# Kernel optimization log

Measured on AMD Instinct MI355X. Metric: run time of the kernel, lower is better.

The kernel has to match this reference:

```python
import jax, jax.numpy as jnp
import numpy as np

BATCH = 2048
DIM = 4096
TEMPERATURE = 0.5
KD_T = 1.0
KD_WEIGHT = 1.0


def setup_inputs() -> dict:
    key = jax.random.key(0)
    k1, k2 = jax.random.split(key)
    emb_target = jax.random.normal(k1, (BATCH, DIM), dtype=jnp.float32)
    emb_surrogate = jax.random.normal(k2, (BATCH, DIM), dtype=jnp.float32)
    return {"emb_target": emb_target, "emb_surrogate": emb_surrogate}


def reference(emb_target, emb_surrogate):
    B = emb_target.shape[0]
    # --- NT-Xent contrastive loss ---
    reps = jnp.concatenate([emb_target, emb_surrogate], axis=0)  # [2B, D]
    # cosine similarity via normalized matmul (eps matches torch cosine_similarity clamp)
    norms = jnp.maximum(jnp.linalg.norm(reps, axis=1, keepdims=True), 1e-8)
    z = reps / norms
    sim = z @ z.T  # [2B, 2B]
    idx = jnp.arange(2 * B)
    # positives: diag offsets +B and -B -> sim[i, (i+B) mod 2B]
    positives = sim[idx, (idx + B) % (2 * B)]  # [2B]
    nominator = jnp.exp(positives / TEMPERATURE)
    neg_mask = 1.0 - jnp.eye(2 * B, dtype=sim.dtype)
    denominator = jnp.sum(neg_mask * jnp.exp(sim / TEMPERATURE), axis=1)  # [2B]
    cont_loss = jnp.sum(-jnp.log(nominator / denominator)) / (2 * B)
    # --- KD softmax-KL ---
    soft_targets = jax.nn.softmax(emb_target / KD_T, axis=-1)
    soft_prob = jax.nn.log_softmax(emb_surrogate / KD_T, axis=-1)
    kd_loss = jnp.sum(soft_targets * (jnp.log(soft_targets) - soft_prob)) / B * KD_T ** 2
    # --- MSE ---
    mse = jnp.mean((emb_surrogate - emb_target) ** 2)
    return cont_loss + KD_WEIGHT * kd_loss + mse
```

## Files before the change

### kernel.cpp

```cpp
#include <hip/hip_runtime.h>
#include <hip/hip_bf16.h>

#define TWO_B 4096
#define DIM_ 4096

typedef __attribute__((ext_vector_type(8))) short bf16x8;
typedef __attribute__((ext_vector_type(4))) float f32x4;
typedef __attribute__((ext_vector_type(4))) int i32x4;

static __device__ __forceinline__ unsigned short f2bf(float x) {
    return __builtin_bit_cast(unsigned short, __float2bfloat16(x));
}

static __device__ __forceinline__ float waveReduceSum(float v) {
    v += __shfl_xor(v, 1);  v += __shfl_xor(v, 2);  v += __shfl_xor(v, 4);
    v += __shfl_xor(v, 8);  v += __shfl_xor(v, 16); v += __shfl_xor(v, 32);
    return v;
}
static __device__ __forceinline__ float waveReduceMax(float v) {
    v = fmaxf(v, __shfl_xor(v, 1));  v = fmaxf(v, __shfl_xor(v, 2));
    v = fmaxf(v, __shfl_xor(v, 4));  v = fmaxf(v, __shfl_xor(v, 8));
    v = fmaxf(v, __shfl_xor(v, 16)); v = fmaxf(v, __shfl_xor(v, 32));
    return v;
}

__global__ __launch_bounds__(256) void row_stats(
    const float* __restrict__ et, const float* __restrict__ es,
    float* __restrict__ rinv, float* __restrict__ qs,
    float* __restrict__ kdp, float* __restrict__ msep,
    float* __restrict__ rowsum, char* __restrict__ z8)
{
    const int b = blockIdx.x;
    const int tid = threadIdx.x;
    const int wid = tid >> 6;

    if (b < 16) rowsum[b * 256 + tid] = 0.f;

    const float4* tp = (const float4*)(et + (size_t)b * DIM_);
    const float4* sp = (const float4*)(es + (size_t)b * DIM_);
    float4 tv[4], sv[4];
#pragma unroll
    for (int i = 0; i < 4; ++i) { tv[i] = tp[tid + 256 * i]; sv[i] = sp[tid + 256 * i]; }

    float mt = -1e30f, ms = -1e30f, amt = 0.f, ams = 0.f;
    float nt2 = 0.f, ns2 = 0.f, msev = 0.f;
#pragma unroll
    for (int i = 0; i < 4; ++i) {
        const float* tx = (const float*)&tv[i];
        const float* sx = (const float*)&sv[i];
#pragma unroll
        for (int j = 0; j < 4; ++j) {
            float a = tx[j], c = sx[j];
            mt = fmaxf(mt, a); ms = fmaxf(ms, c);
            amt = fmaxf(amt, fabsf(a)); ams = fmaxf(ams, fabsf(c));
            nt2 += a * a; ns2 += c * c;
            float d = c - a; msev += d * d;
        }
    }
    mt = waveReduceMax(mt); ms = waveReduceMax(ms);
    amt = waveReduceMax(amt); ams = waveReduceMax(ams);
    __shared__ float smx[4], sms[4], sat[4], sas[4];
    if ((tid & 63) == 0) { smx[wid] = mt; sms[wid] = ms; sat[wid] = amt; sas[wid] = ams; }
    __syncthreads();
    mt = fmaxf(fmaxf(smx[0], smx[1]), fmaxf(smx[2], smx[3]));
    ms = fmaxf(fmaxf(sms[0], sms[1]), fmaxf(sms[2], sms[3]));
    const float maT = fmaxf(fmaxf(fmaxf(sat[0], sat[1]), fmaxf(sat[2], sat[3])), 1e-20f);
    const float maS = fmaxf(fmaxf(fmaxf(sas[0], sas[1]), fmaxf(sas[2], sas[3])), 1e-20f);

    float se_t = 0.f, st = 0.f, sx_ = 0.f, se_s = 0.f;
#pragma unroll
    for (int i = 0; i < 4; ++i) {
        const float* tx = (const float*)&tv[i];
        const float* sx = (const float*)&sv[i];
#pragma unroll
        for (int j = 0; j < 4; ++j) {
            float a = tx[j], c = sx[j];
            float e = __expf(a - mt);
            se_t += e; st += e * a; sx_ += e * c;
            se_s += __expf(c - ms);
        }
    }
    float v0 = waveReduceSum(se_t), v1 = waveReduceSum(st), v2 = waveReduceSum(sx_);
    float v3 = waveReduceSum(se_s), v4 = waveReduceSum(nt2), v5 = waveReduceSum(ns2);
    float v6 = waveReduceSum(msev);
    __shared__ float sred[7][4];
    if ((tid & 63) == 0) {
        sred[0][wid] = v0; sred[1][wid] = v1; sred[2][wid] = v2; sred[3][wid] = v3;
        sred[4][wid] = v4; sred[5][wid] = v5; sred[6][wid] = v6;
    }
    __syncthreads();
    const float rT = sred[4][0] + sred[4][1] + sred[4][2] + sred[4][3];
    const float rS = sred[5][0] + sred[5][1] + sred[5][2] + sred[5][3];
    const float rinvT = 1.f / fmaxf(sqrtf(rT), 1e-8f);
    const float rinvS = 1.f / fmaxf(sqrtf(rS), 1e-8f);

    if (tid == 0) {
        float r0 = sred[0][0] + sred[0][1] + sred[0][2] + sred[0][3];
        float r1 = sred[1][0] + sred[1][1] + sred[1][2] + sred[1][3];
        float r2 = sred[2][0] + sred[2][1] + sred[2][2] + sred[2][3];
        float r3 = sred[3][0] + sred[3][1] + sred[3][2] + sred[3][3];
        float r6 = sred[6][0] + sred[6][1] + sred[6][2] + sred[6][3];
        float lse_t = mt + logf(r0);
        float lse_s = ms + logf(r3);
        kdp[b]  = (r1 - r2) / r0 - lse_t + lse_s;
        msep[b] = r6;
        rinv[b]        = rinvT;
        rinv[b + 2048] = rinvS;
        qs[b]          = maT * rinvT * (1.f / 127.f);
        qs[b + 2048]   = maS * rinvS * (1.f / 127.f);
    }

    if (z8) {
        char* zt = z8 + (size_t)b * DIM_;
        char* zs = z8 + (size_t)(b + 2048) * DIM_;
        const float fT = 127.f / maT, fS = 127.f / maS;
#pragma unroll
        for (int i = 0; i < 4; ++i) {
            const float* tx = (const float*)&tv[i];
            const float* sx = (const float*)&sv[i];
            int pt = 0, ps = 0;
#pragma unroll
            for (int j = 0; j < 4; ++j) {
                int qt = __float2int_rn(tx[j] * fT) & 0xff;
                int qv = __float2int_rn(sx[j] * fS) & 0xff;
                pt |= qt << (8 * j);
                ps |= qv << (8 * j);
            }
            ((int*)zt)[tid + 256 * i] = pt;
            ((int*)zs)[tid + 256 * i] = ps;
        }
    }
}

__global__ __launch_bounds__(256, 2) void cont_gemm12(
    const char* __restrict__ z8, const float* __restrict__ qs,
    float* __restrict__ rowsum, float* __restrict__ pos)
{
    const int bid = blockIdx.x;
    int t = (bid & 7) * 66 + (bid >> 3);
    int bi = 0;
    while (t >= (32 - bi)) { t -= (32 - bi); ++bi; }
    const int bj = bi + t;
    const int brow = bi * 128, bcol = bj * 128;
    const bool dg = (bi == bj);

    __shared__ char As[128 * 128];
    __shared__ char Bs[128 * 128];

    const int tid = threadIdx.x;
    const int lane = tid & 63;
    const int wid = tid >> 6;
    const int wm = wid >> 1, wn = wid & 1;
    const int lrow = lane >> 3;
    const int lblk = lane & 7;

    const char* srcA[4];
    const char* srcB[4];
#pragma unroll
    for (int i = 0; i < 4; ++i) {
        int r = wid * 32 + i * 8 + lrow;
        srcA[i] = z8 + (size_t)(brow + r) * DIM_ + ((lblk ^ lrow) << 4);
        srcB[i] = z8 + (size_t)(bcol + r) * DIM_ + ((lblk ^ lrow) << 4);
    }

    const char* Bbase = dg ? As : Bs;

    i32x4 acc[4][4] = {};

    for (int kt = 0; kt < DIM_; kt += 128) {
        __syncthreads();
#pragma unroll
        for (int i = 0; i < 4; ++i) {
            char* dstA = As + (wid * 32 + i * 8) * 128;
            __builtin_amdgcn_global_load_lds(
                (const __attribute__((address_space(1))) unsigned int*)(srcA[i] + kt),
                (__attribute__((address_space(3))) unsigned int*)dstA, 16, 0, 0);
        }
        if (!dg) {
#pragma unroll
            for (int i = 0; i < 4; ++i) {
                char* dstB = Bs + (wid * 32 + i * 8) * 128;
                __builtin_amdgcn_global_load_lds(
                    (const __attribute__((address_space(1))) unsigned int*)(srcB[i] + kt),
                    (__attribute__((address_space(3))) unsigned int*)dstB, 16, 0, 0);
            }
        }
        __syncthreads();
#pragma unroll
        for (int ks = 0; ks < 2; ++ks) {
            i32x4 af[4], bfr[4];
            const int li = lane & 15;
            const int kb = ks * 64 + (lane >> 4) * 16;
#pragma unroll
            for (int m = 0; m < 4; ++m) {
                int r = wm * 64 + m * 16 + li;
                int off = (r * 128 + kb) ^ ((r & 7) << 4);
                af[m] = *(const i32x4*)(As + off);
            }
#pragma unroll
            for (int n = 0; n < 4; ++n) {
                int r = wn * 64 + n * 16 + li;
                int off = (r * 128 + kb) ^ ((r & 7) << 4);
                bfr[n] = *(const i32x4*)(Bbase + off);
            }
            __builtin_amdgcn_s_setprio(1);
#pragma unroll
            for (int m = 0; m < 4; ++m)
#pragma unroll
                for (int n = 0; n < 4; ++n)
                    acc[m][n] = __builtin_amdgcn_mfma_i32_16x16x64_i8(
                        af[m], bfr[n], acc[m][n], 0, 0, 0);
            __builtin_amdgcn_s_setprio(0);
        }
    }

    const bool posT = (bj == bi + 16);
    const int li = lane & 15;
    const int lg = lane >> 4;
    float sB[4];
#pragma unroll
    for (int n = 0; n < 4; ++n) sB[n] = qs[bcol + wn * 64 + n * 16 + li];
    float cs[4] = {0.f, 0.f, 0.f, 0.f};
#pragma unroll
    for (int m = 0; m < 4; ++m) {
#pragma unroll
        for (int q = 0; q < 4; ++q) {
            int lr = wm * 64 + m * 16 + lg * 4 + q;
            int gr = brow + lr;
            float sA = qs[gr];
            float rsum = 0.f;
#pragma unroll
            for (int n = 0; n < 4; ++n) {
                int gc = bcol + wn * 64 + n * 16 + li;
                float v = (float)acc[m][n][q] * sA * sB[n];
                if (posT && gc == gr + 2048) { pos[gr] = v; pos[gc] = v; }
                float e = (dg && gr == gc) ? 0.f : __expf(2.0f * v);
                rsum += e;
                cs[n] += e;
            }
            rsum += __shfl_xor(rsum, 1);
            rsum += __shfl_xor(rsum, 2);
            rsum += __shfl_xor(rsum, 4);
            rsum += __shfl_xor(rsum, 8);
            if (li == 0) atomicAdd(&rowsum[gr], rsum);
        }
    }
    if (!dg) {
#pragma unroll
        for (int n = 0; n < 4; ++n) {
            float v = cs[n];
            v += __shfl_xor(v, 16);
            v += __shfl_xor(v, 32);
            if (lg == 0) atomicAdd(&rowsum[bcol + wn * 64 + n * 16 + li], v);
        }
    }
}

__global__ __launch_bounds__(256) void cont_gemm(
    const float* __restrict__ et, const float* __restrict__ es,
    const float* __restrict__ rinv, float* __restrict__ rowsum,
    float* __restrict__ pos)
{
    int t = blockIdx.x;
    int bi = 0;
    while (t >= (32 - bi)) { t -= (32 - bi); ++bi; }
    const int bj = bi + t;
    const int brow = bi * 128, bcol = bj * 128;

    __shared__ unsigned short As[128 * 64];
    __shared__ unsigned short Bs[128 * 64];

    const int tid = threadIdx.x;
    const int lane = tid & 63;
    const int wid = tid >> 6;
    const int wm = wid >> 1, wn = wid & 1;

    const int srow = tid >> 4;
    const int sf4 = tid & 15;

    const float* pA[8]; const float* pB[8];
    float riA[8], riB[8];
#pragma unroll
    for (int it = 0; it < 8; ++it) {
        int r = srow + it * 16;
        int ga = brow + r;
        int gb = bcol + r;
        pA[it] = (ga < 2048) ? (et + (size_t)ga * DIM_) : (es + (size_t)(ga - 2048) * DIM_);
        pB[it] = (gb < 2048) ? (et + (size_t)gb * DIM_) : (es + (size_t)(gb - 2048) * DIM_);
        riA[it] = rinv[ga]; riB[it] = rinv[gb];
    }

    f32x4 acc[4][4] = {};

    for (int kt = 0; kt < DIM_; kt += 64) {
        __syncthreads();
#pragma unroll
        for (int it = 0; it < 8; ++it) {
            int r = srow + it * 16;
            int swz = (r & 7) << 4;
            int bo = (r * 128 + sf4 * 8) ^ swz;
            {
                float4 v = *(const float4*)(pA[it] + kt + sf4 * 4);
                float ri = riA[it];
                ushort4 pk = make_ushort4(f2bf(v.x * ri), f2bf(v.y * ri),
                                          f2bf(v.z * ri), f2bf(v.w * ri));
                *(ushort4*)((char*)As + bo) = pk;
            }
            {
                float4 v = *(const float4*)(pB[it] + kt + sf4 * 4);
                float ri = riB[it];
                ushort4 pk = make_ushort4(f2bf(v.x * ri), f2bf(v.y * ri),
                                          f2bf(v.z * ri), f2bf(v.w * ri));
                *(ushort4*)((char*)Bs + bo) = pk;
            }
        }
        __syncthreads();
#pragma unroll
        for (int ks = 0; ks < 2; ++ks) {
            bf16x8 af[4], bfr[4];
            const int li = lane & 15;
            const int kb = ks * 64 + (lane >> 4) * 16;
#pragma unroll
            for (int m = 0; m < 4; ++m) {
                int r = wm * 64 + m * 16 + li;
                int off = (r * 128 + kb) ^ ((r & 7) << 4);
                af[m] = *(const bf16x8*)((const char*)As + off);
            }
#pragma unroll
            for (int n = 0; n < 4; ++n) {
                int r = wn * 64 + n * 16 + li;
                int off = (r * 128 + kb) ^ ((r & 7) << 4);
                bfr[n] = *(const bf16x8*)((const char*)Bs + off);
            }
#pragma unroll
            for (int m = 0; m < 4; ++m)
#pragma unroll
                for (int n = 0; n < 4; ++n)
                    acc[m][n] = __builtin_amdgcn_mfma_f32_16x16x32_bf16(
                        af[m], bfr[n], acc[m][n], 0, 0, 0);
        }
    }

    const bool diag = (bi == bj);
    const bool posT = (bcol == (brow ^ 2048));
    const int li = lane & 15;
    const int lg = lane >> 4;
    float cs[4] = {0.f, 0.f, 0.f, 0.f};
#pragma unroll
    for (int m = 0; m < 4; ++m) {
#pragma unroll
        for (int q = 0; q < 4; ++q) {
            int lr = wm * 64 + m * 16 + lg * 4 + q;
            float rsum = 0.f;
#pragma unroll
            for (int n = 0; n < 4; ++n) {
                int lc = wn * 64 + n * 16 + li;
                float v = acc[m][n][q];
                if (posT && lc == lr) { pos[brow + lr] = v; pos[bcol + lc] = v; }
                float e = (diag && lc == lr) ? 0.f : __expf(2.0f * v);
                rsum += e;
                cs[n] += e;
            }
            rsum += __shfl_xor(rsum, 1);
            rsum += __shfl_xor(rsum, 2);
            rsum += __shfl_xor(rsum, 4);
            rsum += __shfl_xor(rsum, 8);
            if (li == 0) atomicAdd(&rowsum[brow + lr], rsum);
        }
    }
    if (!diag) {
#pragma unroll
        for (int n = 0; n < 4; ++n) {
            float v = cs[n];
            v += __shfl_xor(v, 16);
            v += __shfl_xor(v, 32);
            if (lg == 0) atomicAdd(&rowsum[bcol + wn * 64 + n * 16 + li], v);
        }
    }
}

__global__ __launch_bounds__(256) void finalize(
    const float* __restrict__ rowsum, const float* __restrict__ pos,
    const float* __restrict__ kdp, const float* __restrict__ msep,
    float* __restrict__ out)
{
    const int tid = threadIdx.x;
    float c = 0.f;
    for (int i = tid; i < TWO_B; i += 256)
        c += logf(rowsum[i]) - 2.0f * pos[i];
    float kd = 0.f, ms = 0.f;
    for (int i = tid; i < 2048; i += 256) { kd += kdp[i]; ms += msep[i]; }
    c = waveReduceSum(c); kd = waveReduceSum(kd); ms = waveReduceSum(ms);
    __shared__ float sm[3][4];
    if ((tid & 63) == 0) { sm[0][tid >> 6] = c; sm[1][tid >> 6] = kd; sm[2][tid >> 6] = ms; }
    __syncthreads();
    if (tid == 0) {
        float cont = (sm[0][0] + sm[0][1] + sm[0][2] + sm[0][3]) / 4096.0f;
        float kds  = (sm[1][0] + sm[1][1] + sm[1][2] + sm[1][3]) / 2048.0f;
        float mses = (sm[2][0] + sm[2][1] + sm[2][2] + sm[2][3]) / (2048.0f * 4096.0f);
        out[0] = cont + kds + mses;
    }
}

extern "C" void kernel_launch(void* const* d_in, const int* in_sizes, int n_in,
                              void* d_out, int out_size, void* d_ws, size_t ws_size,
                              hipStream_t stream) {
    const float* et = (const float*)d_in[0];
    const float* es = (const float*)d_in[1];

    const size_t Z_BYTES = (size_t)TWO_B * DIM_;
    const size_t SMALL_FLOATS = 4096 * 4 + 2048 * 2;
    const bool fast = ws_size >= Z_BYTES + SMALL_FLOATS * sizeof(float);

    if (fast) {
        char* z8 = (char*)d_ws;
        float* smallf = (float*)((char*)d_ws + Z_BYTES);
        float* rowsum = smallf;
        float* pos  = smallf + 4096;
        float* qs   = smallf + 4096 * 2;
        float* rinv = smallf + 4096 * 3;
        float* kdp  = smallf + 4096 * 4;
        float* msep = smallf + 4096 * 4 + 2048;
        hipLaunchKernelGGL(row_stats, dim3(2048), dim3(256), 0, stream,
                           et, es, rinv, qs, kdp, msep, rowsum, z8);
        hipLaunchKernelGGL(cont_gemm12, dim3(528), dim3(256), 0, stream, z8, qs, rowsum, pos);
        hipLaunchKernelGGL(finalize, dim3(1), dim3(256), 0, stream, rowsum, pos, kdp, msep, (float*)d_out);
    } else {
        float* ws = (float*)d_ws;
        float* rowsum = ws;
        float* pos  = ws + 4096;
        float* qs   = ws + 4096 * 2;
        float* rinv = ws + 4096 * 3;
        float* kdp  = ws + 4096 * 4;
        float* msep = ws + 4096 * 4 + 2048;
        hipLaunchKernelGGL(row_stats, dim3(2048), dim3(256), 0, stream,
                           et, es, rinv, qs, kdp, msep, rowsum, (char*)nullptr);
        hipLaunchKernelGGL(cont_gemm, dim3(528), dim3(256), 0, stream, et, es, rinv, rowsum, pos);
        hipLaunchKernelGGL(finalize, dim3(1), dim3(256), 0, stream, rowsum, pos, kdp, msep, (float*)d_out);
    }
}
```

Measured before the change: 77.21 us.

## Pair diagonal GEMM tiles into merged blocks for balanced 512-block grid

The int8 similarity GEMM used to launch 528 tiles, 32 of them diagonal tiles that load only one operand. These light tiles are now grouped in pairs: one block loads two adjacent diagonal row-blocks and computes both diagonal products, giving 496 off-diagonal blocks plus 16 merged ones, 512 in total. The aim is to balance work per block and remove the partial wave of a 528-block grid, at the cost of a second accumulator set (more registers) in the merged path. Row_stats also changes to contiguous float4 loads per thread and one int4 store per row, and the fallback path gains a memset.

```diff
diff --git a/kernel.cpp b/kernel.cpp
--- a/kernel.cpp
+++ b/kernel.cpp
@@ -40,7 +40,7 @@
     const float4* sp = (const float4*)(es + (size_t)b * DIM_);
     float4 tv[4], sv[4];
 #pragma unroll
-    for (int i = 0; i < 4; ++i) { tv[i] = tp[tid + 256 * i]; sv[i] = sp[tid + 256 * i]; }
+    for (int i = 0; i < 4; ++i) { tv[i] = tp[tid * 4 + i]; sv[i] = sp[tid * 4 + i]; }
 
     float mt = -1e30f, ms = -1e30f, amt = 0.f, ams = 0.f;
     float nt2 = 0.f, ns2 = 0.f, msev = 0.f;
@@ -111,38 +111,43 @@
     }
 
     if (z8) {
-        char* zt = z8 + (size_t)b * DIM_;
-        char* zs = z8 + (size_t)(b + 2048) * DIM_;
         const float fT = 127.f / maT, fS = 127.f / maS;
+        int4 pt, ps;
+        int* ptp = (int*)&pt; int* psp = (int*)&ps;
 #pragma unroll
         for (int i = 0; i < 4; ++i) {
             const float* tx = (const float*)&tv[i];
             const float* sx = (const float*)&sv[i];
-            int pt = 0, ps = 0;
+            int a = 0, c = 0;
 #pragma unroll
             for (int j = 0; j < 4; ++j) {
-                int qt = __float2int_rn(tx[j] * fT) & 0xff;
-                int qv = __float2int_rn(sx[j] * fS) & 0xff;
-                pt |= qt << (8 * j);
-                ps |= qv << (8 * j);
-            }
-            ((int*)zt)[tid + 256 * i] = pt;
-            ((int*)zs)[tid + 256 * i] = ps;
-        }
-    }
-}
-
-__global__ __launch_bounds__(256, 2) void cont_gemm12(
+                a |= (__float2int_rn(tx[j] * fT) & 0xff) << (8 * j);
+                c |= (__float2int_rn(sx[j] * fS) & 0xff) << (8 * j);
+            }
+            ptp[i] = a; psp[i] = c;
+        }
+        ((int4*)(z8 + (size_t)b * DIM_))[tid] = pt;
+        ((int4*)(z8 + (size_t)(b + 2048) * DIM_))[tid] = ps;
+    }
+}
+
+__global__ __launch_bounds__(256, 2) void cont_gemm14(
     const char* __restrict__ z8, const float* __restrict__ qs,
     float* __restrict__ rowsum, float* __restrict__ pos)
 {
     const int bid = blockIdx.x;
-    int t = (bid & 7) * 66 + (bid >> 3);
-    int bi = 0;
-    while (t >= (32 - bi)) { t -= (32 - bi); ++bi; }
-    const int bj = bi + t;
-    const int brow = bi * 128, bcol = bj * 128;
-    const bool dg = (bi == bj);
+    int t = (bid & 7) * 64 + (bid >> 3);
+
+    int brow, bcol;
+    bool merged;
+    if (t < 496) {
+        int bi = 0;
+        while (t >= (31 - bi)) { t -= (31 - bi); ++bi; }
+        brow = bi * 128; bcol = (bi + 1 + t) * 128; merged = false;
+    } else {
+        int p = t - 496;
+        brow = (2 * p) * 128; bcol = (2 * p + 1) * 128; merged = true;
+    }
 
     __shared__ char As[128 * 128];
     __shared__ char Bs[128 * 128];
@@ -163,9 +168,8 @@
         srcB[i] = z8 + (size_t)(bcol + r) * DIM_ + ((lblk ^ lrow) << 4);
     }
 
-    const char* Bbase = dg ? As : Bs;
-
     i32x4 acc[4][4] = {};
+    i32x4 acc2[4][4] = {};
 
     for (int kt = 0; kt < DIM_; kt += 128) {
         __syncthreads();
@@ -176,14 +180,12 @@
                 (const __attribute__((address_space(1))) unsigned int*)(srcA[i] + kt),
                 (__attribute__((address_space(3))) unsigned int*)dstA, 16, 0, 0);
         }
-        if (!dg) {
-#pragma unroll
-            for (int i = 0; i < 4; ++i) {
-                char* dstB = Bs + (wid * 32 + i * 8) * 128;
-                __builtin_amdgcn_global_load_lds(
-                    (const __attribute__((address_space(1))) unsigned int*)(srcB[i] + kt),
-                    (__attribute__((address_space(3))) unsigned int*)dstB, 16, 0, 0);
-            }
+#pragma unroll
+        for (int i = 0; i < 4; ++i) {
+            char* dstB = Bs + (wid * 32 + i * 8) * 128;
+            __builtin_amdgcn_global_load_lds(
+                (const __attribute__((address_space(1))) unsigned int*)(srcB[i] + kt),
+                (__attribute__((address_space(3))) unsigned int*)dstB, 16, 0, 0);
         }
         __syncthreads();
 #pragma unroll
@@ -201,57 +203,116 @@
             for (int n = 0; n < 4; ++n) {
                 int r = wn * 64 + n * 16 + li;
                 int off = (r * 128 + kb) ^ ((r & 7) << 4);
-                bfr[n] = *(const i32x4*)(Bbase + off);
-            }
-            __builtin_amdgcn_s_setprio(1);
-#pragma unroll
-            for (int m = 0; m < 4; ++m)
-#pragma unroll
-                for (int n = 0; n < 4; ++n)
-                    acc[m][n] = __builtin_amdgcn_mfma_i32_16x16x64_i8(
-                        af[m], bfr[n], acc[m][n], 0, 0, 0);
-            __builtin_amdgcn_s_setprio(0);
-        }
-    }
-
-    const bool posT = (bj == bi + 16);
+                bfr[n] = *(const i32x4*)(Bs + off);
+            }
+            if (!merged) {
+                __builtin_amdgcn_s_setprio(1);
+#pragma unroll
+                for (int m = 0; m < 4; ++m)
+#pragma unroll
+                    for (int n = 0; n < 4; ++n)
+                        acc[m][n] = __builtin_amdgcn_mfma_i32_16x16x64_i8(
+                            af[m], bfr[n], acc[m][n], 0, 0, 0);
+                __builtin_amdgcn_s_setprio(0);
+            } else {
+                i32x4 ca[4], cb[4];
+#pragma unroll
+                for (int n = 0; n < 4; ++n) {
+                    int r = wn * 64 + n * 16 + li;
+                    int off = (r * 128 + kb) ^ ((r & 7) << 4);
+                    ca[n] = *(const i32x4*)(As + off);
+                }
+#pragma unroll
+                for (int m = 0; m < 4; ++m) {
+                    int r = wm * 64 + m * 16 + li;
+                    int off = (r * 128 + kb) ^ ((r & 7) << 4);
+                    cb[m] = *(const i32x4*)(Bs + off);
+                }
+                __builtin_amdgcn_s_setprio(1);
+#pragma unroll
+                for (int m = 0; m < 4; ++m)
+#pragma unroll
+                    for (int n = 0; n < 4; ++n) {
+                        acc[m][n] = __builtin_amdgcn_mfma_i32_16x16x64_i8(
+                            af[m], ca[n], acc[m][n], 0, 0, 0);
+                        acc2[m][n] = __builtin_amdgcn_mfma_i32_16x16x64_i8(
+                            cb[m], bfr[n], acc2[m][n], 0, 0, 0);
+                    }
+                __builtin_amdgcn_s_setprio(0);
+            }
+        }
+    }
+
     const int li = lane & 15;
     const int lg = lane >> 4;
-    float sB[4];
-#pragma unroll
-    for (int n = 0; n < 4; ++n) sB[n] = qs[bcol + wn * 64 + n * 16 + li];
-    float cs[4] = {0.f, 0.f, 0.f, 0.f};
-#pragma unroll
-    for (int m = 0; m < 4; ++m) {
-#pragma unroll
-        for (int q = 0; q < 4; ++q) {
-            int lr = wm * 64 + m * 16 + lg * 4 + q;
-            int gr = brow + lr;
-            float sA = qs[gr];
-            float rsum = 0.f;
-#pragma unroll
-            for (int n = 0; n < 4; ++n) {
-                int gc = bcol + wn * 64 + n * 16 + li;
-                float v = (float)acc[m][n][q] * sA * sB[n];
-                if (posT && gc == gr + 2048) { pos[gr] = v; pos[gc] = v; }
-                float e = (dg && gr == gc) ? 0.f : __expf(2.0f * v);
-                rsum += e;
-                cs[n] += e;
-            }
-            rsum += __shfl_xor(rsum, 1);
-            rsum += __shfl_xor(rsum, 2);
-            rsum += __shfl_xor(rsum, 4);
-            rsum += __shfl_xor(rsum, 8);
-            if (li == 0) atomicAdd(&rowsum[gr], rsum);
-        }
-    }
-    if (!dg) {
+
+    if (!merged) {
+        const bool posT = (bcol == brow + 2048);
+        float sB[4];
+#pragma unroll
+        for (int n = 0; n < 4; ++n) sB[n] = qs[bcol + wn * 64 + n * 16 + li];
+        float cs[4] = {0.f, 0.f, 0.f, 0.f};
+#pragma unroll
+        for (int m = 0; m < 4; ++m) {
+#pragma unroll
+            for (int q = 0; q < 4; ++q) {
+                int lr = wm * 64 + m * 16 + lg * 4 + q;
+                int gr = brow + lr;
+                float sA = qs[gr];
+                float rsum = 0.f;
+#pragma unroll
+                for (int n = 0; n < 4; ++n) {
+                    int gc = bcol + wn * 64 + n * 16 + li;
+                    float v = (float)acc[m][n][q] * sA * sB[n];
+                    if (posT && gc == gr + 2048) { pos[gr] = v; pos[gc] = v; }
+                    float e = __expf(2.0f * v);
+                    rsum += e;
+                    cs[n] += e;
+                }
+                rsum += __shfl_xor(rsum, 1);
+                rsum += __shfl_xor(rsum, 2);
+                rsum += __shfl_xor(rsum, 4);
+                rsum += __shfl_xor(rsum, 8);
+                if (li == 0) atomicAdd(&rowsum[gr], rsum);
+            }
+        }
 #pragma unroll
         for (int n = 0; n < 4; ++n) {
             float v = cs[n];
             v += __shfl_xor(v, 16);
             v += __shfl_xor(v, 32);
             if (lg == 0) atomicAdd(&rowsum[bcol + wn * 64 + n * 16 + li], v);
+        }
+    } else {
+#pragma unroll
+        for (int half = 0; half < 2; ++half) {
+            const int base = half ? bcol : brow;
+            float sB[4];
+#pragma unroll
+            for (int n = 0; n < 4; ++n) sB[n] = qs[base + wn * 64 + n * 16 + li];
+#pragma unroll
+            for (int m = 0; m < 4; ++m) {
+#pragma unroll
+                for (int q = 0; q < 4; ++q) {
+                    int lr = wm * 64 + m * 16 + lg * 4 + q;
+                    int gr = base + lr;
+                    float sA = qs[gr];
+                    float rsum = 0.f;
+#pragma unroll
+                    for (int n = 0; n < 4; ++n) {
+                        int gc = base + wn * 64 + n * 16 + li;
+                        float v = (half ? (float)acc2[m][n][q] : (float)acc[m][n][q])
+                                  * sA * sB[n];
+                        float e = (gr == gc) ? 0.f : __expf(2.0f * v);
+                        rsum += e;
+                    }
+                    rsum += __shfl_xor(rsum, 1);
+                    rsum += __shfl_xor(rsum, 2);
+                    rsum += __shfl_xor(rsum, 4);
+                    rsum += __shfl_xor(rsum, 8);
+                    if (li == 0) atomicAdd(&rowsum[gr], rsum);
+                }
+            }
         }
     }
 }
@@ -423,7 +484,7 @@
         float* msep = smallf + 4096 * 4 + 2048;
         hipLaunchKernelGGL(row_stats, dim3(2048), dim3(256), 0, stream,
                            et, es, rinv, qs, kdp, msep, rowsum, z8);
-        hipLaunchKernelGGL(cont_gemm12, dim3(528), dim3(256), 0, stream, z8, qs, rowsum, pos);
+        hipLaunchKernelGGL(cont_gemm14, dim3(512), dim3(256), 0, stream, z8, qs, rowsum, pos);
         hipLaunchKernelGGL(finalize, dim3(1), dim3(256), 0, stream, rowsum, pos, kdp, msep, (float*)d_out);
     } else {
         float* ws = (float*)d_ws;
@@ -433,6 +494,7 @@
         float* rinv = ws + 4096 * 3;
         float* kdp  = ws + 4096 * 4;
         float* msep = ws + 4096 * 4 + 2048;
+        hipMemsetAsync(rowsum, 0, 4096 * sizeof(float), stream);
         hipLaunchKernelGGL(row_stats, dim3(2048), dim3(256), 0, stream,
                            et, es, rinv, qs, kdp, msep, rowsum, (char*)nullptr);
         hipLaunchKernelGGL(cont_gemm, dim3(528), dim3(256), 0, stream, et, es, rinv, rowsum, pos);
```

New measurement: 160.5 us. 108% more time.

## Use 8-wave blocks for int8 Gram GEMM and vectorize int8 quantized stores

Applied to the files above, without the earlier changes.

The int8 similarity GEMM kernel now runs 512 threads (8 waves in a 2x4 layout) per 128x128 tile instead of 4 waves. Each wave owns a 64x32 subtile, which halves the accumulator registers per wave and should let more waves hide LDS and MFMA latency. The row_stats kernel now loads contiguous float4 chunks per thread and writes the packed int8 rows as a single int4 store. The cost is a larger block and more B-fragment LDS reads per MFMA. A memset is also added to the fallback path.

```diff
diff --git a/kernel.cpp b/kernel.cpp
--- a/kernel.cpp
+++ b/kernel.cpp
@@ -40,7 +40,7 @@
     const float4* sp = (const float4*)(es + (size_t)b * DIM_);
     float4 tv[4], sv[4];
 #pragma unroll
-    for (int i = 0; i < 4; ++i) { tv[i] = tp[tid + 256 * i]; sv[i] = sp[tid + 256 * i]; }
+    for (int i = 0; i < 4; ++i) { tv[i] = tp[tid * 4 + i]; sv[i] = sp[tid * 4 + i]; }
 
     float mt = -1e30f, ms = -1e30f, amt = 0.f, ams = 0.f;
     float nt2 = 0.f, ns2 = 0.f, msev = 0.f;
@@ -111,28 +111,27 @@
     }
 
     if (z8) {
-        char* zt = z8 + (size_t)b * DIM_;
-        char* zs = z8 + (size_t)(b + 2048) * DIM_;
         const float fT = 127.f / maT, fS = 127.f / maS;
+        int4 pt, ps;
+        int* ptp = (int*)&pt; int* psp = (int*)&ps;
 #pragma unroll
         for (int i = 0; i < 4; ++i) {
             const float* tx = (const float*)&tv[i];
             const float* sx = (const float*)&sv[i];
-            int pt = 0, ps = 0;
+            int a = 0, c = 0;
 #pragma unroll
             for (int j = 0; j < 4; ++j) {
-                int qt = __float2int_rn(tx[j] * fT) & 0xff;
-                int qv = __float2int_rn(sx[j] * fS) & 0xff;
-                pt |= qt << (8 * j);
-                ps |= qv << (8 * j);
-            }
-            ((int*)zt)[tid + 256 * i] = pt;
-            ((int*)zs)[tid + 256 * i] = ps;
-        }
-    }
-}
-
-__global__ __launch_bounds__(256, 2) void cont_gemm12(
+                a |= (__float2int_rn(tx[j] * fT) & 0xff) << (8 * j);
+                c |= (__float2int_rn(sx[j] * fS) & 0xff) << (8 * j);
+            }
+            ptp[i] = a; psp[i] = c;
+        }
+        ((int4*)(z8 + (size_t)b * DIM_))[tid] = pt;
+        ((int4*)(z8 + (size_t)(b + 2048) * DIM_))[tid] = ps;
+    }
+}
+
+__global__ __launch_bounds__(512, 4) void cont_gemm16(
     const char* __restrict__ z8, const float* __restrict__ qs,
     float* __restrict__ rowsum, float* __restrict__ pos)
 {
@@ -150,36 +149,40 @@
     const int tid = threadIdx.x;
     const int lane = tid & 63;
     const int wid = tid >> 6;
-    const int wm = wid >> 1, wn = wid & 1;
+    const int wm = wid >> 2;
+    const int wn = wid & 3;
     const int lrow = lane >> 3;
     const int lblk = lane & 7;
-
-    const char* srcA[4];
-    const char* srcB[4];
-#pragma unroll
-    for (int i = 0; i < 4; ++i) {
-        int r = wid * 32 + i * 8 + lrow;
-        srcA[i] = z8 + (size_t)(brow + r) * DIM_ + ((lblk ^ lrow) << 4);
-        srcB[i] = z8 + (size_t)(bcol + r) * DIM_ + ((lblk ^ lrow) << 4);
+    const int li = lane & 15;
+    const int lg = lane >> 4;
+    const int swzc = (lblk ^ lrow) << 4;
+
+    const char* srcA[2];
+    const char* srcB[2];
+#pragma unroll
+    for (int i = 0; i < 2; ++i) {
+        int r = wid * 16 + i * 8 + lrow;
+        srcA[i] = z8 + (size_t)(brow + r) * DIM_ + swzc;
+        srcB[i] = z8 + (size_t)(bcol + r) * DIM_ + swzc;
     }
 
     const char* Bbase = dg ? As : Bs;
 
-    i32x4 acc[4][4] = {};
+    i32x4 acc[4][2] = {};
 
     for (int kt = 0; kt < DIM_; kt += 128) {
         __syncthreads();
 #pragma unroll
-        for (int i = 0; i < 4; ++i) {
-            char* dstA = As + (wid * 32 + i * 8) * 128;
+        for (int i = 0; i < 2; ++i) {
+            char* dstA = As + (wid * 16 + i * 8) * 128;
             __builtin_amdgcn_global_load_lds(
                 (const __attribute__((address_space(1))) unsigned int*)(srcA[i] + kt),
                 (__attribute__((address_space(3))) unsigned int*)dstA, 16, 0, 0);
         }
         if (!dg) {
 #pragma unroll
-            for (int i = 0; i < 4; ++i) {
-                char* dstB = Bs + (wid * 32 + i * 8) * 128;
+            for (int i = 0; i < 2; ++i) {
+                char* dstB = Bs + (wid * 16 + i * 8) * 128;
                 __builtin_amdgcn_global_load_lds(
                     (const __attribute__((address_space(1))) unsigned int*)(srcB[i] + kt),
                     (__attribute__((address_space(3))) unsigned int*)dstB, 16, 0, 0);
@@ -188,8 +191,7 @@
         __syncthreads();
 #pragma unroll
         for (int ks = 0; ks < 2; ++ks) {
-            i32x4 af[4], bfr[4];
-            const int li = lane & 15;
+            i32x4 af[4], bfr[2];
             const int kb = ks * 64 + (lane >> 4) * 16;
 #pragma unroll
             for (int m = 0; m < 4; ++m) {
@@ -198,8 +200,8 @@
                 af[m] = *(const i32x4*)(As + off);
             }
 #pragma unroll
-            for (int n = 0; n < 4; ++n) {
-                int r = wn * 64 + n * 16 + li;
+            for (int n = 0; n < 2; ++n) {
+                int r = wn * 32 + n * 16 + li;
                 int off = (r * 128 + kb) ^ ((r & 7) << 4);
                 bfr[n] = *(const i32x4*)(Bbase + off);
             }
@@ -207,20 +209,18 @@
 #pragma unroll
             for (int m = 0; m < 4; ++m)
 #pragma unroll
-                for (int n = 0; n < 4; ++n)
+                for (int n = 0; n < 2; ++n)
                     acc[m][n] = __builtin_amdgcn_mfma_i32_16x16x64_i8(
                         af[m], bfr[n], acc[m][n], 0, 0, 0);
             __builtin_amdgcn_s_setprio(0);
         }
     }
 
-    const bool posT = (bj == bi + 16);
-    const int li = lane & 15;
-    const int lg = lane >> 4;
-    float sB[4];
-#pragma unroll
-    for (int n = 0; n < 4; ++n) sB[n] = qs[bcol + wn * 64 + n * 16 + li];
-    float cs[4] = {0.f, 0.f, 0.f, 0.f};
+    const bool posT = (bcol == brow + 2048);
+    float sB[2];
+#pragma unroll
+    for (int n = 0; n < 2; ++n) sB[n] = qs[bcol + wn * 32 + n * 16 + li];
+    float cs[2] = {0.f, 0.f};
 #pragma unroll
     for (int m = 0; m < 4; ++m) {
 #pragma unroll
@@ -230,8 +230,8 @@
             float sA = qs[gr];
             float rsum = 0.f;
 #pragma unroll
-            for (int n = 0; n < 4; ++n) {
-                int gc = bcol + wn * 64 + n * 16 + li;
+            for (int n = 0; n < 2; ++n) {
+                int gc = bcol + wn * 32 + n * 16 + li;
                 float v = (float)acc[m][n][q] * sA * sB[n];
                 if (posT && gc == gr + 2048) { pos[gr] = v; pos[gc] = v; }
                 float e = (dg && gr == gc) ? 0.f : __expf(2.0f * v);
@@ -247,11 +247,11 @@
     }
     if (!dg) {
 #pragma unroll
-        for (int n = 0; n < 4; ++n) {
+        for (int n = 0; n < 2; ++n) {
             float v = cs[n];
             v += __shfl_xor(v, 16);
             v += __shfl_xor(v, 32);
-            if (lg == 0) atomicAdd(&rowsum[bcol + wn * 64 + n * 16 + li], v);
+            if (lg == 0) atomicAdd(&rowsum[bcol + wn * 32 + n * 16 + li], v);
         }
     }
 }
@@ -423,7 +423,7 @@
         float* msep = smallf + 4096 * 4 + 2048;
         hipLaunchKernelGGL(row_stats, dim3(2048), dim3(256), 0, stream,
                            et, es, rinv, qs, kdp, msep, rowsum, z8);
-        hipLaunchKernelGGL(cont_gemm12, dim3(528), dim3(256), 0, stream, z8, qs, rowsum, pos);
+        hipLaunchKernelGGL(cont_gemm16, dim3(528), dim3(512), 0, stream, z8, qs, rowsum, pos);
         hipLaunchKernelGGL(finalize, dim3(1), dim3(256), 0, stream, rowsum, pos, kdp, msep, (float*)d_out);
     } else {
         float* ws = (float*)d_ws;
@@ -433,6 +433,7 @@
         float* rinv = ws + 4096 * 3;
         float* kdp  = ws + 4096 * 4;
         float* msep = ws + 4096 * 4 + 2048;
+        hipMemsetAsync(rowsum, 0, 4096 * sizeof(float), stream);
         hipLaunchKernelGGL(row_stats, dim3(2048), dim3(256), 0, stream,
                            et, es, rinv, qs, kdp, msep, rowsum, (char*)nullptr);
         hipLaunchKernelGGL(cont_gemm, dim3(528), dim3(256), 0, stream, et, es, rinv, rowsum, pos);
```

Measured after the change: 109.8 us. 42.2% more time.
